# Kernel optimization log

Hardware: AMD Instinct MI355X
Metric: run time of the kernel (lower is better)

Reference implementation:

```python
import jax, jax.numpy as jnp
import numpy as np
from jax.ops import segment_sum, segment_max

N, D, B = 1536, 32, 8            # nodes, candidate out-degree per node, sequential batch steps
OBS, HID, HEADS, C = 33, 64, 4, 8  # obs_dim, GRU hidden, attn heads, out_dim//heads
E = N * D


def setup_inputs() -> dict:
    key = jax.random.key(0)
    ks = jax.random.split(key, 16)
    g = lambda i, shape, s=0.1: jax.random.normal(ks[i], shape, jnp.float32) * s
    src = jnp.repeat(jnp.arange(N), D)                    # uniform degree -> scatter_topk = row top-k
    dst = jax.random.randint(ks[0], (E,), 0, N)
    return dict(
        H_t=jax.random.normal(ks[1], (B, N, OBS), jnp.float32),
        src=src, dst=dst, k=4,
        W_e1=g(2, (OBS, 32)), b_e1=jnp.zeros(32), W_e2=g(3, (32, 32)), b_e2=jnp.zeros(32),
        ln_g=jnp.ones(32), ln_b=jnp.zeros(32),
        W_ih=g(4, (3 * HID, 32)), W_hh=g(5, (3 * HID, HID)),
        b_ih=jnp.zeros(3 * HID), b_hh=jnp.zeros(3 * HID),
        W_s1=g(6, (2 * HID, 64)), b_s1=jnp.zeros(64), W_s2=g(7, (64, 1)), b_s2=jnp.zeros(1),
        W_gat=g(8, (HID, HEADS * C)), att_src=g(9, (HEADS, C)), att_dst=g(10, (HEADS, C)),
        b_gat=jnp.zeros(HEADS * C),
    )


def _layernorm(x, g, b, eps=1e-5):
    mu = x.mean(-1, keepdims=True)
    var = ((x - mu) ** 2).mean(-1, keepdims=True)
    return (x - mu) * jax.lax.rsqrt(var + eps) * g + b


def _forward(H_t, src, dst, k, W_e1, b_e1, W_e2, b_e2, ln_g, ln_b,
             W_ih, W_hh, b_ih, b_hh, W_s1, b_s1, W_s2, b_s2,
             W_gat, att_src, att_dst, b_gat):
    # ObsEmbedding: Linear-ReLU-Linear-ReLU-LayerNorm, applied to all (B,N) at once
    x = jax.nn.relu(H_t @ W_e1 + b_e1)
    x = jax.nn.relu(x @ W_e2 + b_e2)
    H_emb = _layernorm(x, ln_g, ln_b)              # (B,N,32)

    def step(h, e_t):
        # --- NodeMemory: shared GRUCell, h carried across batch steps ---
        gi = e_t @ W_ih.T + b_ih                   # (N,3H)
        gh = h @ W_hh.T + b_hh
        i_r, i_z, i_n = jnp.split(gi, 3, -1)
        h_r, h_z, h_n = jnp.split(gh, 3, -1)
        r = jax.nn.sigmoid(i_r + h_r)
        z = jax.nn.sigmoid(i_z + h_z)
        n = jnp.tanh(i_n + r * h_n)
        h_new = (1.0 - z) * n + z * h              # (N,HID)

        # --- EdgeScorer: sigmoid MLP score per candidate edge, keep top-k per source ---
        feat = jnp.concatenate([h_new[src], h_new[dst]], -1)        # (E,2*HID)
        score = jax.nn.sigmoid(
            (jax.nn.relu(feat @ W_s1 + b_s1) @ W_s2 + b_s2)[:, 0])  # (E,)
        s2 = score.reshape(N, D)
        top_idx = jax.lax.top_k(s2, k)[1]                           # (N,k)
        keep = (jnp.zeros((N, D), bool)
                .at[jnp.arange(N)[:, None], top_idx].set(True)).reshape(-1)  # (E,)
        w = jnp.where(keep, score, 0.0)                             # soft edge weights

        # --- GATConv (add_self_loops=False), pruned edges masked out of the softmax ---
        xh = (h_new @ W_gat).reshape(N, HEADS, C)
        a_s = (xh * att_src).sum(-1)               # (N,HEADS)
        a_d = (xh * att_dst).sum(-1)
        logit = jax.nn.leaky_relu(a_s[src] + a_d[dst], 0.2)         # (E,HEADS)
        logit = jnp.where(keep[:, None], logit, -1e30)
        m = segment_max(logit, dst, num_segments=N)                 # softmax grouped by target
        ex = jnp.where(keep[:, None], jnp.exp(logit - m[dst]), 0.0)
        ssum = segment_sum(ex, dst, num_segments=N)
        alpha = ex / jnp.clip(ssum[dst], 1e-16)                     # (E,HEADS)

        msg = alpha[:, :, None] * xh[src] * w[:, None, None]        # edge_weight scales messages
        out = segment_sum(msg, dst, num_segments=N).reshape(N, HEADS * C) + b_gat

        # --- densify attention: scatter-accumulate then row-normalize ---
        A = jnp.zeros((HEADS, N, N), alpha.dtype).at[:, src, dst].add(alpha.T)
        A = A / jnp.clip(A.sum(-1, keepdims=True), 1e-9)
        return h_new, (out, A)

    h0 = jnp.zeros((N, HID), H_t.dtype)
    _, (outs, attns) = jax.lax.scan(step, h0, H_emb)
    return outs, attns                              # (B,N,32), (B,HEADS,N,N)


def reference(H_t, src, dst, k, W_e1, b_e1, W_e2, b_e2, ln_g, ln_b,
              W_ih, W_hh, b_ih, b_hh, W_s1, b_s1, W_s2, b_s2,
              W_gat, att_src, att_dst, b_gat):
    return _forward(H_t, src, dst, k, W_e1, b_e1, W_e2, b_e2, ln_g, ln_b,
                    W_ih, W_hh, b_ih, b_hh, W_s1, b_s1, W_s2, b_s2,
                    W_gat, att_src, att_dst, b_gat)
```

## Files before the change

kernel.cpp:

```cpp
#include <hip/hip_runtime.h>
#include <math.h>

#define NN   1536
#define DG   32
#define BB   8
#define OBSD 33
#define HID  64
#define NHEAD 4
#define EE   (NN*DG)
#define MAXDEG 128
#define EMB_BLOCKS (BB*NN/4)
#define GRP_BLOCKS (EE/256)

__device__ __forceinline__ float sigm(float x){ return 1.0f/(1.0f+expf(-x)); }
__device__ __forceinline__ float rl(float v, int l){
    return __int_as_float(__builtin_amdgcn_readlane(__float_as_int(v), l));
}

__global__ void __launch_bounds__(256) k_embgi(
                      const float* __restrict__ Ht,
                      const float* __restrict__ We1, const float* __restrict__ be1,
                      const float* __restrict__ We2, const float* __restrict__ be2,
                      const float* __restrict__ lng, const float* __restrict__ lnb,
                      const float* __restrict__ Wih, const float* __restrict__ bih,
                      float* __restrict__ GI,
                      const int* __restrict__ dst, int* __restrict__ cursor,
                      int* __restrict__ gedge){
    __shared__ float lwih[192*33];
    int tid = threadIdx.x;
    if(blockIdx.x >= EMB_BLOCKS){
        int e = (blockIdx.x - EMB_BLOCKS)*256 + tid;
        if(e<EE){
            int d = dst[e];
            int s = atomicAdd(&cursor[d],1);
            if(s<MAXDEG) gedge[d*MAXDEG+s]=e;
        }
        return;
    }
    for(int i=tid;i<192*32;i+=256){ int r=i>>5, c=i&31; lwih[r*33+c]=Wih[i]; }
    __syncthreads();
    int lane = tid & 63;
    int j32 = lane & 31;
    int bn = blockIdx.x*4 + (tid>>6);
    const float* hrow = Ht + (size_t)bn*OBSD;
    float x1 = be1[j32];
    for(int o=0;o<OBSD;o++) x1 += hrow[o]*We1[o*32+j32];
    x1 = fmaxf(x1,0.f);
    float x2 = be2[j32];
    for(int i=0;i<32;i++) x2 += rl(x1,i) * We2[i*32+j32];
    x2 = fmaxf(x2,0.f);
    float mu = x2;
    for(int m=16;m>=1;m>>=1) mu += __shfl_xor(mu, m, 32);
    mu *= (1.0f/32.0f);
    float d = x2-mu; float var = d*d;
    for(int m=16;m>=1;m>>=1) var += __shfl_xor(var, m, 32);
    var *= (1.0f/32.0f);
    float xln = d*rsqrtf(var+1e-5f)*lng[j32]+lnb[j32];
    int j = lane;
    float gr=bih[j], gz=bih[64+j], gn=bih[128+j];
    for(int kk=0;kk<32;kk++){
        float ek = rl(xln, kk);
        gr += ek*lwih[j*33+kk];
        gz += ek*lwih[(64+j)*33+kk];
        gn += ek*lwih[(128+j)*33+kk];
    }
    float* g = GI + (size_t)bn*192;
    g[j]=gr; g[64+j]=gz; g[128+j]=gn;
}

__global__ void __launch_bounds__(384) k_gru_all(const float* __restrict__ GI,
                       const float* __restrict__ Whh, const float* __restrict__ bhh,
                       float* __restrict__ Hall){
    __shared__ float lw[192*65];
    int tid = threadIdx.x;
    for(int i=tid;i<192*64;i+=384){ int r=i>>6, c=i&63; lw[r*65+c]=Whh[i]; }
    __syncthreads();
    int node = blockIdx.x*6 + (tid>>6);
    int j = tid&63;
    float b_r=bhh[j], b_z=bhh[64+j], b_n=bhh[128+j];
    const float* lwr = lw + j*65;
    const float* lwz = lw + (64+j)*65;
    const float* lwn = lw + (128+j)*65;
    float hold = 0.f;
    for(int t=0;t<BB;t++){
        float hr=b_r, hz=b_z, hn=b_n;
        for(int kk=0;kk<64;kk++){
            float hk = rl(hold,kk);
            hr += hk*lwr[kk];
            hz += hk*lwz[kk];
            hn += hk*lwn[kk];
        }
        const float* g = GI + ((size_t)t*NN+node)*192;
        float r  = sigm(g[j]     + hr);
        float z  = sigm(g[64+j]  + hz);
        float nn_= tanhf(g[128+j] + r*hn);
        hold = (1.f-z)*nn_ + z*hold;
        Hall[((size_t)t*NN+node)*64 + j] = hold;
    }
}

__global__ void __launch_bounds__(256) k_post(const float* __restrict__ Hall,
                       const float* __restrict__ Ws1, const float* __restrict__ Wgat,
                       const float* __restrict__ atts, const float* __restrict__ attd,
                       float* __restrict__ P, float* __restrict__ Q,
                       float* __restrict__ xh, float* __restrict__ as_, float* __restrict__ ad_){
    __shared__ float ws1l[128*64];
    __shared__ float wgl[64*32];
    int tid = threadIdx.x;
    for(int i=tid;i<128*64;i+=256) ws1l[i]=Ws1[i];
    for(int i=tid;i<64*32;i+=256)  wgl[i]=Wgat[i];
    __syncthreads();
    int bn = blockIdx.x*4 + (tid>>6);
    int j = tid&63;
    float hv = Hall[(size_t)bn*64+j];
    float p=0.f,q=0.f,xv=0.f;
    for(int kk=0;kk<64;kk++){
        float hk=rl(hv,kk);
        p += hk*ws1l[kk*64+j];
        q += hk*ws1l[(64+kk)*64+j];
        if(j<32) xv += hk*wgl[kk*32+j];
    }
    P[(size_t)bn*64+j]=p; Q[(size_t)bn*64+j]=q;
    if(j<32){
        xh[(size_t)bn*32+j]=xv;
        float asv = xv*atts[j];
        float adv = xv*attd[j];
        for(int m=1;m<8;m<<=1){ asv += __shfl_xor(asv,m); adv += __shfl_xor(adv,m); }
        if((j&7)==0){ as_[(size_t)bn*4+(j>>3)]=asv; ad_[(size_t)bn*4+(j>>3)]=adv; }
    }
}

__global__ void __launch_bounds__(256) k_edgescore(const float* __restrict__ P, const float* __restrict__ Q,
                       const float* __restrict__ bs1, const float* __restrict__ Ws2,
                       const float* __restrict__ bs2, const int* __restrict__ dst,
                       const int* __restrict__ kptr,
                       const float* __restrict__ as_, const float* __restrict__ ad_,
                       float* __restrict__ rec){
    int t = blockIdx.x;
    int row = blockIdx.y*8 + (threadIdx.x>>5);
    int d = threadIdx.x & 31;
    int e = row*DG + d;
    int de = dst[e];
    const float4* Pr = (const float4*)(P + ((size_t)t*NN+row)*64);
    const float4* Qr = (const float4*)(Q + ((size_t)t*NN+de)*64);
    const float4* B1 = (const float4*)bs1;
    const float4* W2 = (const float4*)Ws2;
    float acc = 0.f;
    #pragma unroll
    for(int jj=0;jj<16;jj++){
        float4 pv=Pr[jj], qv=Qr[jj], bv=B1[jj], wv=W2[jj];
        acc += fmaxf(pv.x+qv.x+bv.x,0.f)*wv.x;
        acc += fmaxf(pv.y+qv.y+bv.y,0.f)*wv.y;
        acc += fmaxf(pv.z+qv.z+bv.z,0.f)*wv.z;
        acc += fmaxf(pv.w+qv.w+bv.w,0.f)*wv.w;
    }
    float score = sigm(acc + bs2[0]);
    int kk = kptr[0]; if(kk>32) kk=32; if(kk<0) kk=0;
    bool sel=false;
    for(int it=0; it<kk; it++){
        float v = sel ? -INFINITY : score;
        int idx = d;
        for(int m=16;m>=1;m>>=1){
            float ov = __shfl_xor(v,m,32);
            int   oi = __shfl_xor(idx,m,32);
            if(ov>v || (ov==v && oi<idx)){ v=ov; idx=oi; }
        }
        if(idx==d) sel=true;
    }
    float wv = sel ? score : 0.f;
    float4 asq = *(const float4*)(as_ + ((size_t)t*NN+row)*4);
    float4 adq = *(const float4*)(ad_ + ((size_t)t*NN+de)*4);
    float ex0,ex1,ex2,ex3;
    {
        float l;
        l = asq.x+adq.x; l = l>0.f ? l : 0.2f*l; ex0 = (wv>0.f)?expf(l):0.f;
        l = asq.y+adq.y; l = l>0.f ? l : 0.2f*l; ex1 = (wv>0.f)?expf(l):0.f;
        l = asq.z+adq.z; l = l>0.f ? l : 0.2f*l; ex2 = (wv>0.f)?expf(l):0.f;
        l = asq.w+adq.w; l = l>0.f ? l : 0.2f*l; ex3 = (wv>0.f)?expf(l):0.f;
    }
    float4* r = (float4*)(rec + ((size_t)t*EE + e)*8);
    r[0] = make_float4(ex0,ex1,ex2,ex3);
    r[1] = make_float4(wv, 0.f, 0.f, 0.f);
}

__global__ void __launch_bounds__(256) k_soft2(const int* __restrict__ gcnt, const int* __restrict__ gedge,
                       const float* __restrict__ rec, const float* __restrict__ xhb,
                       const float* __restrict__ bgat,
                       float* __restrict__ ssum, float* __restrict__ outp){
    int t = blockIdx.x;
    int n = blockIdx.y*4 + (threadIdx.x>>6);
    int lane = threadIdx.x & 63;
    const float* rt   = rec + (size_t)t*EE*8;
    const float* xhbt = xhb + (size_t)t*NN*32;
    int cnt = gcnt[n]; if(cnt>MAXDEG) cnt=MAXDEG;
    const int* ge = gedge + (size_t)n*MAXDEG;

    int   e0=0, e1=0;
    float w0=0.f, w1=0.f;
    float4 x0v = make_float4(0,0,0,0), x1v = make_float4(0,0,0,0);
    bool h0v = lane < cnt, h1v = 64+lane < cnt;
    if(h0v){
        e0 = ge[lane];
        const float4* r = (const float4*)(rt + (size_t)e0*8);
        x0v = r[0]; w0 = r[1].x;
    }
    if(h1v){
        e1 = ge[64+lane];
        const float4* r = (const float4*)(rt + (size_t)e1*8);
        x1v = r[0]; w1 = r[1].x;
    }
    float ss[4] = { x0v.x+x1v.x, x0v.y+x1v.y, x0v.z+x1v.z, x0v.w+x1v.w };
    #pragma unroll
    for(int mm=32;mm>=1;mm>>=1){
        #pragma unroll
        for(int h=0;h<4;h++) ss[h] += __shfl_xor(ss[h], mm);
    }
    float inv[4];
    #pragma unroll
    for(int h=0;h<4;h++) inv[h] = 1.0f/fmaxf(ss[h],1e-16f);

    float acc[32];
    #pragma unroll
    for(int c=0;c<32;c++) acc[c]=0.f;

    if(h0v && w0>0.f){
        const float4* xr4 = (const float4*)(xhbt + (size_t)(e0>>5)*32);
        float a0[4] = { x0v.x*inv[0], x0v.y*inv[1], x0v.z*inv[2], x0v.w*inv[3] };
        #pragma unroll
        for(int h=0;h<4;h++){
            float aw = a0[h]*w0;
            float4 xa = xr4[h*2], xb = xr4[h*2+1];
            acc[h*8+0]+=aw*xa.x; acc[h*8+1]+=aw*xa.y; acc[h*8+2]+=aw*xa.z; acc[h*8+3]+=aw*xa.w;
            acc[h*8+4]+=aw*xb.x; acc[h*8+5]+=aw*xb.y; acc[h*8+6]+=aw*xb.z; acc[h*8+7]+=aw*xb.w;
        }
    }
    if(h1v && w1>0.f){
        const float4* xr4 = (const float4*)(xhbt + (size_t)(e1>>5)*32);
        float a1[4] = { x1v.x*inv[0], x1v.y*inv[1], x1v.z*inv[2], x1v.w*inv[3] };
        #pragma unroll
        for(int h=0;h<4;h++){
            float aw = a1[h]*w1;
            float4 xa = xr4[h*2], xb = xr4[h*2+1];
            acc[h*8+0]+=aw*xa.x; acc[h*8+1]+=aw*xa.y; acc[h*8+2]+=aw*xa.z; acc[h*8+3]+=aw*xa.w;
            acc[h*8+4]+=aw*xb.x; acc[h*8+5]+=aw*xb.y; acc[h*8+6]+=aw*xb.z; acc[h*8+7]+=aw*xb.w;
        }
    }
    #pragma unroll
    for(int mm=32;mm>=1;mm>>=1){
        #pragma unroll
        for(int c=0;c<32;c++) acc[c] += __shfl_xor(acc[c], mm);
    }
    if(lane==0){
        *(float4*)(ssum + ((size_t)t*NN+n)*4) = make_float4(ss[0],ss[1],ss[2],ss[3]);
        float4* o = (float4*)(outp + ((size_t)t*NN+n)*32);
        const float4* bg4 = (const float4*)bgat;
        #pragma unroll
        for(int q8=0;q8<8;q8++){
            float4 b = bg4[q8];
            o[q8] = make_float4(acc[q8*4]+b.x, acc[q8*4+1]+b.y, acc[q8*4+2]+b.z, acc[q8*4+3]+b.w);
        }
    }
}

__global__ void __launch_bounds__(256) k_scatter(const float* __restrict__ rec,
                       const float* __restrict__ ssum,
                       const int* __restrict__ dst, float* __restrict__ attn){
    __shared__ float rowbuf[NHEAD][NN];
    __shared__ float rs[NHEAD];
    __shared__ float rsf[NHEAD];
    int t = blockIdx.x;
    int n = blockIdx.y;
    int tid = threadIdx.x;
    for(int i=tid;i<NHEAD*(NN/4);i+=256) ((float4*)rowbuf)[i]=make_float4(0.f,0.f,0.f,0.f);
    if(tid<NHEAD) rs[tid]=0.f;
    __syncthreads();
    float a=0.f; int de=0; int h=0;
    if(tid<128){
        int d = tid>>2; h = tid&3;
        int e = n*DG+d;
        float ex = rec[((size_t)t*EE + e)*8 + h];
        de = dst[e];
        if(ex>0.f){
            float ssv = ssum[((size_t)t*NN+de)*4 + h];
            a = ex / fmaxf(ssv, 1e-16f);
            atomicAdd(&rs[h], a);
        }
    }
    __syncthreads();
    if(tid<NHEAD) rsf[tid] = 1.0f/fmaxf(rs[tid],1e-9f);
    __syncthreads();
    if(tid<128 && a>0.f) atomicAdd(&rowbuf[h][de], a*rsf[h]);
    __syncthreads();
    size_t tb = (size_t)t*NHEAD*NN*NN;
    for(int i=tid;i<NHEAD*(NN/4);i+=256){
        int hh = i/(NN/4); int c4 = i%(NN/4);
        float4 v = ((const float4*)rowbuf[hh])[c4];
        ((float4*)(attn + tb + (size_t)hh*NN*NN + (size_t)n*NN))[c4] = v;
    }
}

extern "C" void kernel_launch(void* const* d_in, const int* in_sizes, int n_in,
                              void* d_out, int out_size, void* d_ws, size_t ws_size,
                              hipStream_t stream) {
    const float* Ht   = (const float*)d_in[0];
    const int*   src  = (const int*)  d_in[1];
    const int*   dst  = (const int*)  d_in[2];
    const int*   kptr = (const int*)  d_in[3];
    const float* We1  = (const float*)d_in[4];
    const float* be1  = (const float*)d_in[5];
    const float* We2  = (const float*)d_in[6];
    const float* be2  = (const float*)d_in[7];
    const float* lng  = (const float*)d_in[8];
    const float* lnb  = (const float*)d_in[9];
    const float* Wih  = (const float*)d_in[10];
    const float* Whh  = (const float*)d_in[11];
    const float* bih  = (const float*)d_in[12];
    const float* bhh  = (const float*)d_in[13];
    const float* Ws1  = (const float*)d_in[14];
    const float* bs1  = (const float*)d_in[15];
    const float* Ws2  = (const float*)d_in[16];
    const float* bs2  = (const float*)d_in[17];
    const float* Wgat = (const float*)d_in[18];
    const float* atts = (const float*)d_in[19];
    const float* attd = (const float*)d_in[20];
    const float* bgat = (const float*)d_in[21];
    (void)src;

    float* outp = (float*)d_out;
    float* attn = outp + (size_t)BB*NN*32;

    float* ws    = (float*)d_ws;
    float* GI    = ws;
    float* Hall  = ws + 2359296;
    float* P     = ws + 3145728;
    float* Q     = ws + 3932160;
    float* xh    = ws + 4718592;
    float* as_   = ws + 5111808;
    float* ad_   = ws + 5160960;
    float* ssum  = ws + 5210112;
    float* rec   = ws + 5259264;
    int*   ibase = (int*)(ws + 8404992);
    int*   cursor= ibase;
    int*   gedge = ibase + 2048;

    hipMemsetAsync(cursor, 0, (size_t)NN*sizeof(int), stream);

    k_embgi<<<EMB_BLOCKS+GRP_BLOCKS, 256, 0, stream>>>(Ht, We1, be1, We2, be2, lng, lnb,
                                                       Wih, bih, GI, dst, cursor, gedge);
    k_gru_all<<<NN/6, 384, 0, stream>>>(GI, Whh, bhh, Hall);
    k_post<<<BB*NN/4, 256, 0, stream>>>(Hall, Ws1, Wgat, atts, attd, P, Q, xh, as_, ad_);
    {
        dim3 g(BB, NN/8);
        k_edgescore<<<g, 256, 0, stream>>>(P, Q, bs1, Ws2, bs2, dst, kptr, as_, ad_, rec);
    }
    {
        dim3 gs(BB, NN/4);
        k_soft2<<<gs, 256, 0, stream>>>(cursor, gedge, rec, xh, bgat, ssum, outp);
        dim3 g(BB, NN);
        k_scatter<<<g, 256, 0, stream>>>(rec, ssum, dst, attn);
    }
}
```

Baseline: 465.8 us.

## Parallelize edge scoring over hidden dim with one block per source row

The edge scorer now uses one block per (step, source row) instead of one thread per edge. Each lane owns one hidden feature and reads coalesced Q rows for 8 edges, and scores are reduced with wave shuffles into shared memory. A single 32-lane group then does the top-k and writes a ballot keep-mask, and the output record is written by 8 threads per edge. This replaces the strided per-thread float4 loads of full 64-wide P/Q rows, at the cost of 8x more blocks, two barriers, and a serial top-k on a fraction of the block.

```diff
diff --git a/kernel.cpp b/kernel.cpp
--- a/kernel.cpp
+++ b/kernel.cpp
@@ -136,51 +136,69 @@
                        const int* __restrict__ kptr,
                        const float* __restrict__ as_, const float* __restrict__ ad_,
                        float* __restrict__ rec){
+    __shared__ float sc[DG];
+    __shared__ int   dsl[DG];
+    __shared__ unsigned int keepm;
     int t = blockIdx.x;
-    int row = blockIdx.y*8 + (threadIdx.x>>5);
-    int d = threadIdx.x & 31;
+    int row = blockIdx.y;
+    int tid = threadIdx.x;
+    int wv = tid>>6;
+    int j  = tid&63;
+    float pj  = P[((size_t)t*NN+row)*64 + j];
+    float b1j = bs1[j];
+    float w2j = Ws2[j];
+    const int ebase = row*DG + wv*8;
+    int   de[8];
+    float qv[8];
+    #pragma unroll
+    for(int i=0;i<8;i++){
+        de[i] = dst[ebase+i];
+        qv[i] = Q[((size_t)t*NN+de[i])*64 + j];
+    }
+    #pragma unroll
+    for(int i=0;i<8;i++){
+        float v = fmaxf(pj + qv[i] + b1j, 0.f) * w2j;
+        #pragma unroll
+        for(int m=32;m>=1;m>>=1) v += __shfl_xor(v, m);
+        if(j==0){ sc[wv*8+i] = v; dsl[wv*8+i] = de[i]; }
+    }
+    __syncthreads();
+    if(tid < 32){
+        float score = sigm(sc[tid] + bs2[0]);
+        sc[tid] = score;
+        int kk = kptr[0]; if(kk>32) kk=32; if(kk<0) kk=0;
+        bool sel=false;
+        for(int it=0; it<kk; it++){
+            float v = sel ? -INFINITY : score;
+            int idx = tid;
+            for(int m=16;m>=1;m>>=1){
+                float ov = __shfl_xor(v,m,32);
+                int   oi = __shfl_xor(idx,m,32);
+                if(ov>v || (ov==v && oi<idx)){ v=ov; idx=oi; }
+            }
+            if(idx==tid) sel=true;
+        }
+        unsigned int ballot = (unsigned int)(__ballot(sel) & 0xffffffffull);
+        if(tid==0) keepm = ballot;
+    }
+    __syncthreads();
+    int d = tid>>3, f = tid&7;
     int e = row*DG + d;
-    int de = dst[e];
-    const float4* Pr = (const float4*)(P + ((size_t)t*NN+row)*64);
-    const float4* Qr = (const float4*)(Q + ((size_t)t*NN+de)*64);
-    const float4* B1 = (const float4*)bs1;
-    const float4* W2 = (const float4*)Ws2;
-    float acc = 0.f;
-    #pragma unroll
-    for(int jj=0;jj<16;jj++){
-        float4 pv=Pr[jj], qv=Qr[jj], bv=B1[jj], wv=W2[jj];
-        acc += fmaxf(pv.x+qv.x+bv.x,0.f)*wv.x;
-        acc += fmaxf(pv.y+qv.y+bv.y,0.f)*wv.y;
-        acc += fmaxf(pv.z+qv.z+bv.z,0.f)*wv.z;
-        acc += fmaxf(pv.w+qv.w+bv.w,0.f)*wv.w;
-    }
-    float score = sigm(acc + bs2[0]);
-    int kk = kptr[0]; if(kk>32) kk=32; if(kk<0) kk=0;
-    bool sel=false;
-    for(int it=0; it<kk; it++){
-        float v = sel ? -INFINITY : score;
-        int idx = d;
-        for(int m=16;m>=1;m>>=1){
-            float ov = __shfl_xor(v,m,32);
-            int   oi = __shfl_xor(idx,m,32);
-            if(ov>v || (ov==v && oi<idx)){ v=ov; idx=oi; }
-        }
-        if(idx==d) sel=true;
-    }
-    float wv = sel ? score : 0.f;
-    float4 asq = *(const float4*)(as_ + ((size_t)t*NN+row)*4);
-    float4 adq = *(const float4*)(ad_ + ((size_t)t*NN+de)*4);
-    float ex0,ex1,ex2,ex3;
-    {
-        float l;
-        l = asq.x+adq.x; l = l>0.f ? l : 0.2f*l; ex0 = (wv>0.f)?expf(l):0.f;
-        l = asq.y+adq.y; l = l>0.f ? l : 0.2f*l; ex1 = (wv>0.f)?expf(l):0.f;
-        l = asq.z+adq.z; l = l>0.f ? l : 0.2f*l; ex2 = (wv>0.f)?expf(l):0.f;
-        l = asq.w+adq.w; l = l>0.f ? l : 0.2f*l; ex3 = (wv>0.f)?expf(l):0.f;
-    }
-    float4* r = (float4*)(rec + ((size_t)t*EE + e)*8);
-    r[0] = make_float4(ex0,ex1,ex2,ex3);
-    r[1] = make_float4(wv, 0.f, 0.f, 0.f);
+    float wval = ((keepm>>d)&1u) ? sc[d] : 0.f;
+    float out;
+    if(f < 4){
+        int dei = dsl[(d&~7)] ;
+        dei = dsl[d];
+        float asv = as_[((size_t)t*NN+row)*4 + f];
+        float adv = ad_[((size_t)t*NN+dei)*4 + f];
+        float l = asv + adv; l = l>0.f ? l : 0.2f*l;
+        out = (wval>0.f) ? expf(l) : 0.f;
+    } else if(f == 4){
+        out = wval;
+    } else {
+        out = 0.f;
+    }
+    rec[((size_t)t*EE + e)*8 + f] = out;
 }
 
 __global__ void __launch_bounds__(256) k_soft2(const int* __restrict__ gcnt, const int* __restrict__ gedge,
@@ -350,7 +368,7 @@
     k_gru_all<<<NN/6, 384, 0, stream>>>(GI, Whh, bhh, Hall);
     k_post<<<BB*NN/4, 256, 0, stream>>>(Hall, Ws1, Wgat, atts, attd, P, Q, xh, as_, ad_);
     {
-        dim3 g(BB, NN/8);
+        dim3 g(BB, NN);
         k_edgescore<<<g, 256, 0, stream>>>(P, Q, bs1, Ws2, bs2, dst, kptr, as_, ad_, rec);
     }
     {
```

Result: slower. 482.1 us (+3.5%).
